# Optimization experiments

Hardware: AMD Instinct MI355X
Metric: run time of the kernel (lower is better)

The kernel has to match this reference:

```python
import jax, jax.numpy as jnp
import numpy as np

N = 100000        # num nodes
E = 1600000       # num edges
IN_DIM = 256
HID = 64          # per-head out_dim
OUT_DIM = 256
H = 4             # num heads
EDGE_DIM = 16
NEG_SLOPE = 0.2

def _xavier(key, shape):
    fan_in, fan_out = shape[-2], shape[-1]
    bound = float(np.sqrt(6.0 / (fan_in + fan_out)))
    return jax.random.uniform(key, shape, jnp.float32, -bound, bound)

def setup_inputs() -> dict:
    key = jax.random.key(0)
    ks = jax.random.split(key, 8)
    x = jax.random.normal(ks[0], (N, IN_DIM), jnp.float32)
    edge_index = jax.random.randint(ks[1], (2, E), 0, N, jnp.int64)
    edge_attr = jax.random.normal(ks[2], (E, EDGE_DIM), jnp.float32)
    W = _xavier(ks[3], (H, IN_DIM, HID))
    W_edge = _xavier(ks[4], (H, EDGE_DIM, HID))
    att = _xavier(ks[5], (H, 3 * HID, 1))[..., 0]          # [H, 3*HID]
    proj_w = _xavier(ks[6], (H * HID, OUT_DIM))
    proj_b = jnp.zeros((OUT_DIM,), jnp.float32)
    return {"x": x, "edge_index": edge_index, "edge_attr": edge_attr,
            "W": W, "W_edge": W_edge, "att": att,
            "proj_w": proj_w, "proj_b": proj_b}

def reference(x, edge_index, edge_attr, W, W_edge, att, proj_w, proj_b):
    src = edge_index[0]  # x_j (source) indices
    dst = edge_index[1]  # x_i (target) indices; softmax/aggregation segments

    # Per-head node transform: [H, N, HID]
    xw = jnp.einsum('ni,hio->hno', x, W)
    x_i = xw[:, dst]                                  # [H, E, HID]
    x_j = xw[:, src]                                  # [H, E, HID]
    edge_proj = jnp.einsum('ed,hdo->heo', edge_attr, W_edge)  # [H, E, HID]

    a1, a2, a3 = att[:, :HID], att[:, HID:2*HID], att[:, 2*HID:]  # [H, HID] each
    e = (jnp.einsum('heo,ho->he', x_i, a1)
         + jnp.einsum('heo,ho->he', x_j, a2)
         + jnp.einsum('heo,ho->he', edge_proj, a3))   # [H, E]
    e = jnp.where(e >= 0, e, NEG_SLOPE * e)           # LeakyReLU

    def seg_softmax(eh):  # eh: [E]
        m = jax.ops.segment_max(eh, dst, num_segments=N)
        m = jnp.where(jnp.isfinite(m), m, 0.0)
        ex = jnp.exp(eh - m[dst])
        s = jax.ops.segment_sum(ex, dst, num_segments=N)
        return ex / (s[dst] + 1e-16)

    alpha = jax.vmap(seg_softmax)(e)                  # [H, E]  (dropout: eval mode)

    msg = x_j * alpha[..., None]                      # [H, E, HID]
    out_h = jax.vmap(lambda m: jax.ops.segment_sum(m, dst, num_segments=N))(msg)  # [H, N, HID]
    out = jnp.transpose(out_h, (1, 0, 2)).reshape(N, H * HID)  # concat heads
    out = out @ proj_w + proj_b
    return jax.nn.elu(out)
```

## Files before the change

kernel.cpp:

```cpp
#include <hip/hip_runtime.h>
#include <hip/hip_bf16.h>
#include <stdint.h>

#define N_NODES 100000
#define E_EDGES 1600000
#define NEG_SLOPE 0.2f
#define NBUCK 1563
#define BK_SH 6
#define CAP 2048

typedef short short8 __attribute__((ext_vector_type(8)));
typedef float f32x4 __attribute__((ext_vector_type(4)));

__device__ __forceinline__ unsigned short f2bf(float f) {
  union { float f; unsigned int u; } c; c.f = f;
  unsigned int u = c.u;
  unsigned int r = u + 0x7FFFu + ((u >> 16) & 1u);
  return (unsigned short)(r >> 16);
}
__device__ __forceinline__ float asf(unsigned int u) {
  union { unsigned int u; float f; } c; c.u = u;
  return c.f;
}

__global__ void k_detect(const void* ei, int* flag) {
  int t = threadIdx.x;
  int v = ((const int*)ei)[2 * t + 1];
  unsigned long long b = __ballot(v != 0);
  if (t == 0) *flag = (b != 0ull) ? 1 : 0;
}

__global__ void k_prep(const float* __restrict__ W, const float* __restrict__ proj_w,
                       const float* __restrict__ W_edge, const float* __restrict__ att,
                       unsigned short* __restrict__ Bt, unsigned short* __restrict__ Pt,
                       float* __restrict__ w3) {
  int t = blockIdx.x * 256 + threadIdx.x;
  if (t < 65536) {
    int col = t >> 8, k = t & 255;
    int h = col >> 6, o = col & 63;
    Bt[t] = f2bf(W[h * 16384 + k * 64 + o]);
  } else if (t < 131072) {
    int t2 = t - 65536;
    int o = t2 >> 8, i = t2 & 255;
    Pt[t2] = f2bf(proj_w[i * 256 + o]);
  } else if (t < 131136) {
    int t3 = t - 131072;
    int h = t3 >> 4, d = t3 & 15;
    float s = 0.f;
    for (int o = 0; o < 64; ++o)
      s += W_edge[h * 1024 + d * 64 + o] * att[h * 192 + 128 + o];
    w3[t3] = s;
  }
}

__global__ __launch_bounds__(256, 4) void k_gemm_x(const float* __restrict__ x,
    const unsigned short* __restrict__ Bt, const float* __restrict__ att,
    unsigned short* __restrict__ xwb, float* __restrict__ s1, float* __restrict__ s2) {
  __shared__ unsigned short As[16384];
  const int bm = blockIdx.x * 64;
  const int t = threadIdx.x;

#pragma unroll
  for (int i = 0; i < 16; ++i) {
    int c = i * 256 + t;
    int row = c >> 6, f4 = c & 63;
    uint2 w = make_uint2(0u, 0u);
    if (bm + row < N_NODES) {
      float4 v = *(const float4*)(x + (size_t)(bm + row) * 256 + f4 * 4);
      w.x = (unsigned int)f2bf(v.x) | ((unsigned int)f2bf(v.y) << 16);
      w.y = (unsigned int)f2bf(v.z) | ((unsigned int)f2bf(v.w) << 16);
    }
    int phys = row * 512 + (((f4 >> 1) ^ (row & 7)) << 4) + ((f4 & 1) << 3);
    *(uint2*)((char*)As + phys) = w;
  }
  __syncthreads();

  const int wave = t >> 6;
  const int lane = t & 63;
  const int l16 = lane & 15, lg = lane >> 4;
  const int colbase = wave * 64;
  f32x4 acc[4][4];
#pragma unroll
  for (int i = 0; i < 4; i++)
#pragma unroll
    for (int j = 0; j < 4; j++) acc[i][j] = (f32x4){0.f, 0.f, 0.f, 0.f};

  for (int ks = 0; ks < 8; ++ks) {
    const int k0 = ks * 32 + lg * 8;
    short8 a[4], b[4];
#pragma unroll
    for (int mi = 0; mi < 4; mi++) {
      int row = mi * 16 + l16;
      int phys = row * 512 + (((ks * 4 + lg) ^ (row & 7)) << 4);
      a[mi] = *(const short8*)((const char*)As + phys);
    }
#pragma unroll
    for (int ni = 0; ni < 4; ni++) {
      int col = colbase + ni * 16 + l16;
      b[ni] = *(const short8*)(Bt + col * 256 + k0);
    }
#pragma unroll
    for (int mi = 0; mi < 4; mi++)
#pragma unroll
      for (int ni = 0; ni < 4; ni++)
        acc[mi][ni] = __builtin_amdgcn_mfma_f32_16x16x32_bf16(a[mi], b[ni], acc[mi][ni], 0, 0, 0);
  }

  float a1v[4], a2v[4];
#pragma unroll
  for (int ni = 0; ni < 4; ni++) {
    a1v[ni] = att[wave * 192 + ni * 16 + l16];
    a2v[ni] = att[wave * 192 + 64 + ni * 16 + l16];
  }
#pragma unroll
  for (int mi = 0; mi < 4; mi++) {
#pragma unroll
    for (int r = 0; r < 4; r++) {
      int row = bm + mi * 16 + lg * 4 + r;
      float p1 = 0.f, p2 = 0.f;
#pragma unroll
      for (int ni = 0; ni < 4; ni++) {
        float v = acc[mi][ni][r];
        p1 += v * a1v[ni];
        p2 += v * a2v[ni];
      }
#pragma unroll
      for (int m = 1; m < 16; m <<= 1) {
        p1 += __shfl_xor(p1, m, 64);
        p2 += __shfl_xor(p2, m, 64);
      }
      if (row < N_NODES) {
#pragma unroll
        for (int ni = 0; ni < 4; ni++) {
          int col = colbase + ni * 16 + l16;
          xwb[(size_t)row * 256 + col] = f2bf(acc[mi][ni][r]);
        }
        if (l16 == 0) {
          s1[row * 4 + wave] = p1;
          s2[row * 4 + wave] = p2;
        }
      }
    }
  }
}

__global__ __launch_bounds__(256) void k_quant(const unsigned short* __restrict__ xwb,
    unsigned int* __restrict__ xwq, float* __restrict__ scl) {
  int n = blockIdx.x * 4 + (threadIdx.x >> 6);
  if (n >= N_NODES) return;
  int lane = threadIdx.x & 63;
  uint2 u = *(const uint2*)(xwb + (size_t)n * 256 + lane * 4);
  float f0 = asf(u.x << 16), f1 = asf(u.x & 0xFFFF0000u);
  float f2 = asf(u.y << 16), f3 = asf(u.y & 0xFFFF0000u);
  float m = fmaxf(fmaxf(fabsf(f0), fabsf(f1)), fmaxf(fabsf(f2), fabsf(f3)));
#pragma unroll
  for (int off = 1; off < 64; off <<= 1) m = fmaxf(m, __shfl_xor(m, off, 64));
  m += 1e-30f;
  float inv = 127.f / m;
  int q0 = __float2int_rn(f0 * inv);
  int q1 = __float2int_rn(f1 * inv);
  int q2 = __float2int_rn(f2 * inv);
  int q3 = __float2int_rn(f3 * inv);
  unsigned int pk = (q0 & 0xFF) | ((q1 & 0xFF) << 8) | ((q2 & 0xFF) << 16) |
                    ((unsigned int)(q3 & 0xFF) << 24);
  xwq[(size_t)n * 64 + lane] = pk;
  if (lane == 0) scl[n] = m * (1.f / 127.f);
}

__global__ __launch_bounds__(1024) void k_hist(const void* ei, const int* __restrict__ flag,
                                               int* __restrict__ bhist) {
  __shared__ int h[NBUCK];
  for (int i = threadIdx.x; i < NBUCK; i += 1024) h[i] = 0;
  __syncthreads();
  int f = *flag;
  int base = blockIdx.x * 4096;
#pragma unroll
  for (int k = 0; k < 4; ++k) {
    int e = base + k * 1024 + threadIdx.x;
    if (e < E_EDGES) {
      int dst = f ? ((const int*)ei)[E_EDGES + e] : (int)(((const long long*)ei)[E_EDGES + e]);
      atomicAdd(&h[dst >> BK_SH], 1);
    }
  }
  __syncthreads();
  for (int i = threadIdx.x; i < NBUCK; i += 1024) {
    int c = h[i];
    if (c) atomicAdd(&bhist[i], c);
  }
}

__global__ __launch_bounds__(1024) void k_scanb(const int* __restrict__ bhist,
                                                int* __restrict__ boff, int* __restrict__ bcur) {
  __shared__ int s[2048];
  int t = threadIdx.x;
  int ia = t, ib = t + 1024;
  int va = (ia < NBUCK) ? bhist[ia] : 0;
  int vb = (ib < NBUCK) ? bhist[ib] : 0;
  s[ia] = va; s[ib] = vb;
  __syncthreads();
  for (int off = 1; off < 2048; off <<= 1) {
    int xa = (ia >= off) ? s[ia - off] : 0;
    int xb = (ib >= off) ? s[ib - off] : 0;
    __syncthreads();
    s[ia] += xa; s[ib] += xb;
    __syncthreads();
  }
  if (ia < NBUCK) { boff[ia] = s[ia] - va; bcur[ia] = s[ia] - va; }
  if (ib < NBUCK) { boff[ib] = s[ib] - vb; bcur[ib] = s[ib] - vb; }
  if (t == 0) boff[NBUCK] = E_EDGES;
}

__global__ __launch_bounds__(1024) void k_edge(const void* ei, const int* __restrict__ flag,
                       const float* __restrict__ edge_attr,
                       const float* __restrict__ s1, const float* __restrict__ s2,
                       const float* __restrict__ w3g, int* __restrict__ bcur,
                       uint4* __restrict__ evs) {
  __shared__ float w3[64];
  __shared__ int cnt[NBUCK];
  __shared__ int rb[NBUCK];
  __shared__ int cur[NBUCK];
  const int t = threadIdx.x;
  for (int i = t; i < NBUCK; i += 1024) { cnt[i] = 0; cur[i] = 0; }
  if (t < 64) w3[t] = w3g[t];
  __syncthreads();

  const int f = *flag;
  const int base = blockIdx.x * 4096;
  int dstv[4], srcv[4];
  unsigned int pav[4], pbv[4];
#pragma unroll
  for (int k = 0; k < 4; ++k) {
    int e = base + k * 1024 + t;
    dstv[k] = -1;
    if (e < E_EDGES) {
      int src, dst;
      if (f) {
        src = ((const int*)ei)[e];
        dst = ((const int*)ei)[E_EDGES + e];
      } else {
        src = (int)(((const long long*)ei)[e]);
        dst = (int)(((const long long*)ei)[E_EDGES + e]);
      }
      float4 sd = *(const float4*)(s1 + (size_t)dst * 4);
      float4 ss = *(const float4*)(s2 + (size_t)src * 4);
      float ea[16];
#pragma unroll
      for (int i = 0; i < 4; i++) {
        float4 v = *(const float4*)(edge_attr + (size_t)e * 16 + i * 4);
        ea[4 * i] = v.x; ea[4 * i + 1] = v.y; ea[4 * i + 2] = v.z; ea[4 * i + 3] = v.w;
      }
      float ex[4];
#pragma unroll
      for (int h = 0; h < 4; h++) {
        float d = 0.f;
#pragma unroll
        for (int i = 0; i < 16; i++) d += ea[i] * w3[h * 16 + i];
        float v = (&sd.x)[h] + (&ss.x)[h] + d;
        v = (v >= 0.f) ? v : NEG_SLOPE * v;
        ex[h] = __expf(v);
      }
      dstv[k] = dst;
      srcv[k] = src;
      pav[k] = ((unsigned int)f2bf(ex[1]) << 16) | (unsigned int)f2bf(ex[0]);
      pbv[k] = ((unsigned int)f2bf(ex[3]) << 16) | (unsigned int)f2bf(ex[2]);
      atomicAdd(&cnt[dst >> BK_SH], 1);
    }
  }
  __syncthreads();
  for (int i = t; i < NBUCK; i += 1024) {
    int c = cnt[i];
    if (c) rb[i] = atomicAdd(&bcur[i], c);
  }
  __syncthreads();
#pragma unroll
  for (int k = 0; k < 4; ++k) {
    if (dstv[k] >= 0) {
      int bk = dstv[k] >> BK_SH;
      int pos = rb[bk] + atomicAdd(&cur[bk], 1);
      evs[pos] = make_uint4((unsigned int)srcv[k], pav[k], pbv[k],
                            (unsigned int)(dstv[k] & 63));
    }
  }
}

__global__ __launch_bounds__(256) void k_aggr(const int* __restrict__ boff,
    const uint4* __restrict__ evs, const unsigned int* __restrict__ xwq,
    const float* __restrict__ scl, unsigned short* __restrict__ out_hb) {
  __shared__ int lsrc[CAP];
  __shared__ uint2 lw[CAP];
  __shared__ int cnt[64], bs[64], cur[64];
  const int b = blockIdx.x;
  const int t = threadIdx.x;
  const int e0 = boff[b];
  const int ne = boff[b + 1] - e0;
  if (t < 64) { cnt[t] = 0; cur[t] = 0; }
  __syncthreads();
  const bool ok = (ne <= CAP);
  if (ok) {
    uint4 rv[8];
#pragma unroll
    for (int k = 0; k < 8; ++k) {
      int i = k * 256 + t;
      if (i < ne) {
        rv[k] = evs[e0 + i];
        atomicAdd(&cnt[rv[k].w], 1);
      }
    }
    __syncthreads();
    if (t < 64) bs[t] = cnt[t];
    __syncthreads();
    for (int off = 1; off < 64; off <<= 1) {
      int x = 0;
      if (t < 64 && t >= off) x = bs[t - off];
      __syncthreads();
      if (t < 64) bs[t] += x;
      __syncthreads();
    }
#pragma unroll
    for (int k = 0; k < 8; ++k) {
      int i = k * 256 + t;
      if (i < ne) {
        int ld = rv[k].w;
        int slot = bs[ld] - cnt[ld] + atomicAdd(&cur[ld], 1);
        lsrc[slot] = (int)rv[k].x;
        lw[slot] = make_uint2(rv[k].y, rv[k].z);
      }
    }
    __syncthreads();
  }

  const int wv = t >> 6, lane = t & 63;
  const int hsel = lane >> 4;
  const bool hlo2 = (hsel < 2);
  const bool hodd = (hsel & 1);

#define EDGE_FMA(wv_, sc_, u_)                                            \
  {                                                                       \
    unsigned int wp = hlo2 ? (wv_).x : (wv_).y;                           \
    float wlo = asf(wp << 16), whi = asf(wp & 0xFFFF0000u);               \
    float w = hodd ? whi : wlo;                                           \
    den += w;                                                             \
    float ws = w * (sc_);                                                 \
    acc0 += ws * (float)(int)(signed char)((u_) & 0xFF);                  \
    acc1 += ws * (float)(int)(signed char)(((u_) >> 8) & 0xFF);           \
    acc2 += ws * (float)(int)(signed char)(((u_) >> 16) & 0xFF);          \
    acc3 += ws * (float)(int)(signed char)((u_) >> 24);                   \
  }

  for (int r = 0; r < 16; ++r) {
    const int ln = wv * 16 + r;
    const int n = b * 64 + ln;
    if (n >= N_NODES) break;
    float acc0 = 0.f, acc1 = 0.f, acc2 = 0.f, acc3 = 0.f, den = 0.f;
    if (ok) {
      const int je = bs[ln];
      int j = je - cnt[ln];
      for (; j + 4 <= je; j += 4) {
        int s0 = lsrc[j], s1_ = lsrc[j + 1], s2_ = lsrc[j + 2], s3_ = lsrc[j + 3];
        uint2 w0 = lw[j], w1 = lw[j + 1], w2 = lw[j + 2], w3_ = lw[j + 3];
        float c0 = scl[s0], c1 = scl[s1_], c2 = scl[s2_], c3 = scl[s3_];
        unsigned int u0 = xwq[(size_t)s0 * 64 + lane];
        unsigned int u1 = xwq[(size_t)s1_ * 64 + lane];
        unsigned int u2 = xwq[(size_t)s2_ * 64 + lane];
        unsigned int u3 = xwq[(size_t)s3_ * 64 + lane];
        EDGE_FMA(w0, c0, u0);
        EDGE_FMA(w1, c1, u1);
        EDGE_FMA(w2, c2, u2);
        EDGE_FMA(w3_, c3, u3);
      }
      for (; j < je; ++j) {
        int s0 = lsrc[j];
        uint2 w0 = lw[j];
        float c0 = scl[s0];
        unsigned int u0 = xwq[(size_t)s0 * 64 + lane];
        EDGE_FMA(w0, c0, u0);
      }
    } else {
      for (int i = 0; i < ne; ++i) {
        uint4 v0 = evs[e0 + i];
        if ((int)v0.w == ln) {
          uint2 w0 = make_uint2(v0.y, v0.z);
          float c0 = scl[v0.x];
          unsigned int u0 = xwq[(size_t)v0.x * 64 + lane];
          EDGE_FMA(w0, c0, u0);
        }
      }
    }
    float d = den + 1e-16f;
    uint2 o;
    o.x = ((unsigned int)f2bf(acc1 / d) << 16) | (unsigned int)f2bf(acc0 / d);
    o.y = ((unsigned int)f2bf(acc3 / d) << 16) | (unsigned int)f2bf(acc2 / d);
    *(uint2*)(out_hb + (size_t)n * 256 + lane * 4) = o;
  }
#undef EDGE_FMA
}

__global__ __launch_bounds__(256, 4) void k_gemm_out(const unsigned short* __restrict__ A,
    const unsigned short* __restrict__ Pt, const float* __restrict__ bias,
    float* __restrict__ out) {
  __shared__ unsigned short As[16384];
  const int bm = blockIdx.x * 64;
  const int t = threadIdx.x;

#pragma unroll
  for (int i = 0; i < 8; ++i) {
    int c = i * 256 + t;
    int row = c >> 5, G = c & 31;
    short8 v = (short8){0, 0, 0, 0, 0, 0, 0, 0};
    if (bm + row < N_NODES) v = *(const short8*)(A + (size_t)(bm + row) * 256 + G * 8);
    int phys = row * 512 + ((G ^ (row & 7)) << 4);
    *(short8*)((char*)As + phys) = v;
  }
  __syncthreads();

  const int wave = t >> 6;
  const int lane = t & 63;
  const int l16 = lane & 15, lg = lane >> 4;
  const int colbase = wave * 64;
  f32x4 acc[4][4];
#pragma unroll
  for (int i = 0; i < 4; i++)
#pragma unroll
    for (int j = 0; j < 4; j++) acc[i][j] = (f32x4){0.f, 0.f, 0.f, 0.f};

  for (int ks = 0; ks < 8; ++ks) {
    const int k0 = ks * 32 + lg * 8;
    short8 a[4], b[4];
#pragma unroll
    for (int mi = 0; mi < 4; mi++) {
      int row = mi * 16 + l16;
      int phys = row * 512 + (((ks * 4 + lg) ^ (row & 7)) << 4);
      a[mi] = *(const short8*)((const char*)As + phys);
    }
#pragma unroll
    for (int ni = 0; ni < 4; ni++) {
      int col = colbase + ni * 16 + l16;
      b[ni] = *(const short8*)(Pt + col * 256 + k0);
    }
#pragma unroll
    for (int mi = 0; mi < 4; mi++)
#pragma unroll
      for (int ni = 0; ni < 4; ni++)
        acc[mi][ni] = __builtin_amdgcn_mfma_f32_16x16x32_bf16(a[mi], b[ni], acc[mi][ni], 0, 0, 0);
  }
#pragma unroll
  for (int mi = 0; mi < 4; mi++) {
#pragma unroll
    for (int r = 0; r < 4; r++) {
      int row = bm + mi * 16 + lg * 4 + r;
      if (row < N_NODES) {
#pragma unroll
        for (int ni = 0; ni < 4; ni++) {
          int col = colbase + ni * 16 + l16;
          float v = acc[mi][ni][r] + bias[col];
          v = (v > 0.f) ? v : expm1f(v);
          out[(size_t)row * 256 + col] = v;
        }
      }
    }
  }
}

extern "C" void kernel_launch(void* const* d_in, const int* in_sizes, int n_in,
                              void* d_out, int out_size, void* d_ws, size_t ws_size,
                              hipStream_t stream) {
  const float* x = (const float*)d_in[0];
  const void* ei = d_in[1];
  const float* edge_attr = (const float*)d_in[2];
  const float* W = (const float*)d_in[3];
  const float* W_edge = (const float*)d_in[4];
  const float* att = (const float*)d_in[5];
  const float* proj_w = (const float*)d_in[6];
  const float* proj_b = (const float*)d_in[7];
  float* out = (float*)d_out;

  char* ws = (char*)d_ws;
  size_t off = 0;
  auto alloc = [&](size_t bytes) -> void* {
    void* p = (void*)(ws + off);
    off += (bytes + 255) & ~(size_t)255;
    return p;
  };
  unsigned short* xwb   = (unsigned short*)alloc((size_t)N_NODES * 256 * 2);
  unsigned int* xwq     = (unsigned int*)alloc((size_t)N_NODES * 256);
  float* scl     = (float*)alloc((size_t)N_NODES * 4);
  unsigned short* outhb = (unsigned short*)alloc((size_t)N_NODES * 256 * 2);
  float* s1      = (float*)alloc((size_t)N_NODES * 4 * 4);
  float* s2      = (float*)alloc((size_t)N_NODES * 4 * 4);
  uint4* evs     = (uint4*)alloc((size_t)E_EDGES * 16);
  int* bhist     = (int*)alloc((size_t)NBUCK * 4);
  int* boff      = (int*)alloc((size_t)(NBUCK + 1) * 4);
  int* bcur      = (int*)alloc((size_t)NBUCK * 4);
  unsigned short* Bt = (unsigned short*)alloc(65536 * 2);
  unsigned short* Pt = (unsigned short*)alloc(65536 * 2);
  float* w3      = (float*)alloc(64 * 4);
  int* flag      = (int*)alloc(256);

  const int NB_E = (E_EDGES + 4095) / 4096;

  hipMemsetAsync(bhist, 0, (size_t)NBUCK * 4, stream);
  k_detect<<<1, 64, 0, stream>>>(ei, flag);
  k_prep<<<(131136 + 255) / 256, 256, 0, stream>>>(W, proj_w, W_edge, att, Bt, Pt, w3);
  k_gemm_x<<<(N_NODES + 63) / 64, 256, 0, stream>>>(x, Bt, att, xwb, s1, s2);
  k_quant<<<(N_NODES + 3) / 4, 256, 0, stream>>>(xwb, xwq, scl);
  k_hist<<<NB_E, 1024, 0, stream>>>(ei, flag, bhist);
  k_scanb<<<1, 1024, 0, stream>>>(bhist, boff, bcur);
  k_edge<<<NB_E, 1024, 0, stream>>>(ei, flag, edge_attr, s1, s2, w3, bcur, evs);
  k_aggr<<<NBUCK, 256, 0, stream>>>(boff, evs, xwq, scl, outhb);
  k_gemm_out<<<(N_NODES + 63) / 64, 256, 0, stream>>>(outhb, Pt, proj_b, out);
}
```

Before: 352.0 us.

## Fuse int8 quantization into node GEMM epilogue with per-head scales

```diff
diff --git a/kernel.cpp b/kernel.cpp
--- a/kernel.cpp
+++ b/kernel.cpp
@@ -7,7 +7,7 @@
 #define NEG_SLOPE 0.2f
 #define NBUCK 1563
 #define BK_SH 6
-#define CAP 2048
+#define CAP 1536
 
 typedef short short8 __attribute__((ext_vector_type(8)));
 typedef float f32x4 __attribute__((ext_vector_type(4)));
@@ -42,7 +42,8 @@
   } else if (t < 131072) {
     int t2 = t - 65536;
     int o = t2 >> 8, i = t2 & 255;
-    Pt[t2] = f2bf(proj_w[i * 256 + o]);
+    int orig = (i >> 6) * 64 + ((i >> 2) & 15) + 16 * (i & 3);
+    Pt[t2] = f2bf(proj_w[orig * 256 + o]);
   } else if (t < 131136) {
     int t3 = t - 131072;
     int h = t3 >> 4, d = t3 & 15;
@@ -55,7 +56,8 @@
 
 __global__ __launch_bounds__(256, 4) void k_gemm_x(const float* __restrict__ x,
     const unsigned short* __restrict__ Bt, const float* __restrict__ att,
-    unsigned short* __restrict__ xwb, float* __restrict__ s1, float* __restrict__ s2) {
+    unsigned int* __restrict__ xwq, float* __restrict__ scl4,
+    float* __restrict__ s1, float* __restrict__ s2) {
   __shared__ unsigned short As[16384];
   const int bm = blockIdx.x * 64;
   const int t = threadIdx.x;
@@ -117,54 +119,34 @@
 #pragma unroll
     for (int r = 0; r < 4; r++) {
       int row = bm + mi * 16 + lg * 4 + r;
-      float p1 = 0.f, p2 = 0.f;
-#pragma unroll
-      for (int ni = 0; ni < 4; ni++) {
-        float v = acc[mi][ni][r];
-        p1 += v * a1v[ni];
-        p2 += v * a2v[ni];
-      }
+      float a0 = acc[mi][0][r], a1 = acc[mi][1][r], a2 = acc[mi][2][r], a3 = acc[mi][3][r];
+      float p1 = a0 * a1v[0] + a1 * a1v[1] + a2 * a1v[2] + a3 * a1v[3];
+      float p2 = a0 * a2v[0] + a1 * a2v[1] + a2 * a2v[2] + a3 * a2v[3];
+      float mx = fmaxf(fmaxf(fabsf(a0), fabsf(a1)), fmaxf(fabsf(a2), fabsf(a3)));
 #pragma unroll
       for (int m = 1; m < 16; m <<= 1) {
         p1 += __shfl_xor(p1, m, 64);
         p2 += __shfl_xor(p2, m, 64);
+        mx = fmaxf(mx, __shfl_xor(mx, m, 64));
       }
       if (row < N_NODES) {
-#pragma unroll
-        for (int ni = 0; ni < 4; ni++) {
-          int col = colbase + ni * 16 + l16;
-          xwb[(size_t)row * 256 + col] = f2bf(acc[mi][ni][r]);
-        }
+        mx += 1e-30f;
+        float inv = 127.f / mx;
+        int q0 = __float2int_rn(a0 * inv);
+        int q1 = __float2int_rn(a1 * inv);
+        int q2 = __float2int_rn(a2 * inv);
+        int q3 = __float2int_rn(a3 * inv);
+        unsigned int pk = (q0 & 0xFF) | ((q1 & 0xFF) << 8) | ((q2 & 0xFF) << 16) |
+                          ((unsigned int)(q3 & 0xFF) << 24);
+        xwq[(size_t)row * 64 + wave * 16 + l16] = pk;
         if (l16 == 0) {
           s1[row * 4 + wave] = p1;
           s2[row * 4 + wave] = p2;
+          scl4[row * 4 + wave] = mx * (1.f / 127.f);
         }
       }
     }
   }
-}
-
-__global__ __launch_bounds__(256) void k_quant(const unsigned short* __restrict__ xwb,
-    unsigned int* __restrict__ xwq, float* __restrict__ scl) {
-  int n = blockIdx.x * 4 + (threadIdx.x >> 6);
-  if (n >= N_NODES) return;
-  int lane = threadIdx.x & 63;
-  uint2 u = *(const uint2*)(xwb + (size_t)n * 256 + lane * 4);
-  float f0 = asf(u.x << 16), f1 = asf(u.x & 0xFFFF0000u);
-  float f2 = asf(u.y << 16), f3 = asf(u.y & 0xFFFF0000u);
-  float m = fmaxf(fmaxf(fabsf(f0), fabsf(f1)), fmaxf(fabsf(f2), fabsf(f3)));
-#pragma unroll
-  for (int off = 1; off < 64; off <<= 1) m = fmaxf(m, __shfl_xor(m, off, 64));
-  m += 1e-30f;
-  float inv = 127.f / m;
-  int q0 = __float2int_rn(f0 * inv);
-  int q1 = __float2int_rn(f1 * inv);
-  int q2 = __float2int_rn(f2 * inv);
-  int q3 = __float2int_rn(f3 * inv);
-  unsigned int pk = (q0 & 0xFF) | ((q1 & 0xFF) << 8) | ((q2 & 0xFF) << 16) |
-                    ((unsigned int)(q3 & 0xFF) << 24);
-  xwq[(size_t)n * 64 + lane] = pk;
-  if (lane == 0) scl[n] = m * (1.f / 127.f);
 }
 
 __global__ __launch_bounds__(1024) void k_hist(const void* ei, const int* __restrict__ flag,
@@ -285,7 +267,7 @@
 
 __global__ __launch_bounds__(256) void k_aggr(const int* __restrict__ boff,
     const uint4* __restrict__ evs, const unsigned int* __restrict__ xwq,
-    const float* __restrict__ scl, unsigned short* __restrict__ out_hb) {
+    const float* __restrict__ scl4, unsigned short* __restrict__ out_hb) {
   __shared__ int lsrc[CAP];
   __shared__ uint2 lw[CAP];
   __shared__ int cnt[64], bs[64], cur[64];
@@ -297,9 +279,9 @@
   __syncthreads();
   const bool ok = (ne <= CAP);
   if (ok) {
-    uint4 rv[8];
-#pragma unroll
-    for (int k = 0; k < 8; ++k) {
+    uint4 rv[6];
+#pragma unroll
+    for (int k = 0; k < 6; ++k) {
       int i = k * 256 + t;
       if (i < ne) {
         rv[k] = evs[e0 + i];
@@ -317,7 +299,7 @@
       __syncthreads();
     }
 #pragma unroll
-    for (int k = 0; k < 8; ++k) {
+    for (int k = 0; k < 6; ++k) {
       int i = k * 256 + t;
       if (i < ne) {
         int ld = rv[k].w;
@@ -358,7 +340,10 @@
       for (; j + 4 <= je; j += 4) {
         int s0 = lsrc[j], s1_ = lsrc[j + 1], s2_ = lsrc[j + 2], s3_ = lsrc[j + 3];
         uint2 w0 = lw[j], w1 = lw[j + 1], w2 = lw[j + 2], w3_ = lw[j + 3];
-        float c0 = scl[s0], c1 = scl[s1_], c2 = scl[s2_], c3 = scl[s3_];
+        float c0 = scl4[(size_t)s0 * 4 + hsel];
+        float c1 = scl4[(size_t)s1_ * 4 + hsel];
+        float c2 = scl4[(size_t)s2_ * 4 + hsel];
+        float c3 = scl4[(size_t)s3_ * 4 + hsel];
         unsigned int u0 = xwq[(size_t)s0 * 64 + lane];
         unsigned int u1 = xwq[(size_t)s1_ * 64 + lane];
         unsigned int u2 = xwq[(size_t)s2_ * 64 + lane];
@@ -371,7 +356,7 @@
       for (; j < je; ++j) {
         int s0 = lsrc[j];
         uint2 w0 = lw[j];
-        float c0 = scl[s0];
+        float c0 = scl4[(size_t)s0 * 4 + hsel];
         unsigned int u0 = xwq[(size_t)s0 * 64 + lane];
         EDGE_FMA(w0, c0, u0);
       }
@@ -380,7 +365,7 @@
         uint4 v0 = evs[e0 + i];
         if ((int)v0.w == ln) {
           uint2 w0 = make_uint2(v0.y, v0.z);
-          float c0 = scl[v0.x];
+          float c0 = scl4[(size_t)v0.x * 4 + hsel];
           unsigned int u0 = xwq[(size_t)v0.x * 64 + lane];
           EDGE_FMA(w0, c0, u0);
         }
@@ -481,9 +466,8 @@
     off += (bytes + 255) & ~(size_t)255;
     return p;
   };
-  unsigned short* xwb   = (unsigned short*)alloc((size_t)N_NODES * 256 * 2);
   unsigned int* xwq     = (unsigned int*)alloc((size_t)N_NODES * 256);
-  float* scl     = (float*)alloc((size_t)N_NODES * 4);
+  float* scl4    = (float*)alloc((size_t)N_NODES * 4 * 4);
   unsigned short* outhb = (unsigned short*)alloc((size_t)N_NODES * 256 * 2);
   float* s1      = (float*)alloc((size_t)N_NODES * 4 * 4);
   float* s2      = (float*)alloc((size_t)N_NODES * 4 * 4);
@@ -501,11 +485,10 @@
   hipMemsetAsync(bhist, 0, (size_t)NBUCK * 4, stream);
   k_detect<<<1, 64, 0, stream>>>(ei, flag);
   k_prep<<<(131136 + 255) / 256, 256, 0, stream>>>(W, proj_w, W_edge, att, Bt, Pt, w3);
-  k_gemm_x<<<(N_NODES + 63) / 64, 256, 0, stream>>>(x, Bt, att, xwb, s1, s2);
-  k_quant<<<(N_NODES + 3) / 4, 256, 0, stream>>>(xwb, xwq, scl);
+  k_gemm_x<<<(N_NODES + 63) / 64, 256, 0, stream>>>(x, Bt, att, xwq, scl4, s1, s2);
   k_hist<<<NB_E, 1024, 0, stream>>>(ei, flag, bhist);
   k_scanb<<<1, 1024, 0, stream>>>(bhist, boff, bcur);
   k_edge<<<NB_E, 1024, 0, stream>>>(ei, flag, edge_attr, s1, s2, w3, bcur, evs);
-  k_aggr<<<NBUCK, 256, 0, stream>>>(boff, evs, xwq, scl, outhb);
+  k_aggr<<<NBUCK, 256, 0, stream>>>(boff, evs, xwq, scl4, outhb);
   k_gemm_out<<<(N_NODES + 63) / 64, 256, 0, stream>>>(outhb, Pt, proj_b, out);
 }
```

Result: faster. 325.3 us (-7.6%).
